# Optimization experiments

Measured on AMD Instinct MI355X. Metric: run time of the kernel, lower is better.

## Reference

```python
import jax, jax.numpy as jnp
import numpy as np


def setup_inputs() -> dict:
    key = jax.random.key(0)
    k1, k2 = jax.random.split(key)
    B, C, L = 64, 36, 4096
    x0 = jax.random.normal(k1, (B, C, L), dtype=jnp.float32)
    y0 = jax.random.normal(k2, (B, C, L), dtype=jnp.float32)
    return {"x0": x0, "y0": y0}


def reference(x0, y0):
    # Original torch code:
    #   result1 = (1/L) * sum_{i=0}^{L-1} roll(x0, i, dim=2) * y0
    #   result2 = (1/L) * sum_{i=0}^{L-1} roll(y0, i, dim=2) * y0
    # At each output position l, summing roll(x,i)[...,l] over all L shifts
    # visits every position of x exactly once, so the shift-sum equals the
    # full sum over the last axis. The loop is therefore mathematically
    # identical to:
    #   result1 = y0 * mean(x0, axis=-1, keepdims=True)
    #   result2 = y0 * mean(y0, axis=-1, keepdims=True)
    # which we compute in one fused pass (bit-for-bit same math up to
    # floating-point summation order).
    mean_x = jnp.mean(x0, axis=-1, keepdims=True)  # [B,C,1]
    mean_y = jnp.mean(y0, axis=-1, keepdims=True)  # [B,C,1]
    result = y0 * (mean_x + mean_y)                # [B,C,L]
    return result
```

## Files before the change

kernel.cpp:

```cpp
#include <hip/hip_runtime.h>
#include <stdint.h>


#define LL     4096
#define ROWS   (64 * 36)
#define BLOCK  64
#define F4LANE (LL / 4 / 64)

__global__ __launch_bounds__(BLOCK) void spo2_rowscale(
    const float* __restrict__ x,
    const float* __restrict__ y,
    float* __restrict__ out)
{
    const int lane = threadIdx.x;
    const size_t base = (size_t)blockIdx.x * LL;

    const float4* xv = (const float4*)(x + base);
    const float4* yv = (const float4*)(y + base);
    float4*       ov = (float4*)(out + base);

    float4 yr[F4LANE];
#pragma unroll
    for (int i = 0; i < F4LANE; ++i)
        yr[i] = yv[lane + i * 64];

    float sx0 = 0.f, sx1 = 0.f, sx2 = 0.f, sx3 = 0.f;
#pragma unroll
    for (int i = 0; i < F4LANE; i += 4) {
        float4 a = xv[lane + (i + 0) * 64];
        float4 b = xv[lane + (i + 1) * 64];
        float4 c = xv[lane + (i + 2) * 64];
        float4 d = xv[lane + (i + 3) * 64];
        sx0 += a.x + a.y + a.z + a.w;
        sx1 += b.x + b.y + b.z + b.w;
        sx2 += c.x + c.y + c.z + c.w;
        sx3 += d.x + d.y + d.z + d.w;
    }
    float s = (sx0 + sx1) + (sx2 + sx3);

    float sy0 = 0.f, sy1 = 0.f;
#pragma unroll
    for (int i = 0; i < F4LANE; i += 2) {
        sy0 += yr[i].x + yr[i].y + yr[i].z + yr[i].w;
        sy1 += yr[i + 1].x + yr[i + 1].y + yr[i + 1].z + yr[i + 1].w;
    }
    s += sy0 + sy1;

#pragma unroll
    for (int off = 32; off > 0; off >>= 1)
        s += __shfl_xor(s, off, 64);

    const float scale = s * (1.0f / (float)LL);

#pragma unroll
    for (int i = 0; i < F4LANE; ++i) {
        float4 o;
        o.x = yr[i].x * scale;
        o.y = yr[i].y * scale;
        o.z = yr[i].z * scale;
        o.w = yr[i].w * scale;
        ov[lane + i * 64] = o;
    }
}

extern "C" void kernel_launch(void* const* d_in, const int* in_sizes, int n_in,
                              void* d_out, int out_size, void* d_ws, size_t ws_size,
                              hipStream_t stream) {
    const float* x = (const float*)d_in[0];
    const float* y = (const float*)d_in[1];
    float* out = (float*)d_out;
    spo2_rowscale<<<ROWS, BLOCK, 0, stream>>>(x, y, out);
}
```

Baseline: 108.8 us.

## Use 256-thread blocks per row with LDS cross-wave reduction and nontemporal stores

Each row is now handled by four wavefronts (256 threads) instead of one, so each thread holds 4 float4s of x and y in registers instead of 16. A shared-memory step combines the per-wave partial sums, and the outputs are written with nontemporal stores. The intent is more memory-level parallelism and occupancy for this bandwidth-bound kernel, with less cache pollution from the output. In exchange it adds a __syncthreads and an LDS round trip per block.

```diff
diff --git a/kernel.cpp b/kernel.cpp
--- a/kernel.cpp
+++ b/kernel.cpp
@@ -2,64 +2,58 @@
 #include <stdint.h>
 
 
-#define LL     4096
-#define ROWS   (64 * 36)
-#define BLOCK  64
-#define F4LANE (LL / 4 / 64)
+typedef float v4f __attribute__((ext_vector_type(4)));
 
-__global__ __launch_bounds__(BLOCK) void spo2_rowscale(
+#define LL    4096
+#define ROWS  (64 * 36)
+#define BLOCK 256
+#define F4T   (LL / 4 / BLOCK)
+
+__global__ __launch_bounds__(BLOCK, 8) void spo2_rowscale(
     const float* __restrict__ x,
     const float* __restrict__ y,
     float* __restrict__ out)
 {
-    const int lane = threadIdx.x;
+    const int tid  = threadIdx.x;
     const size_t base = (size_t)blockIdx.x * LL;
 
-    const float4* xv = (const float4*)(x + base);
-    const float4* yv = (const float4*)(y + base);
-    float4*       ov = (float4*)(out + base);
+    const v4f* xv = (const v4f*)(x + base);
+    const v4f* yv = (const v4f*)(y + base);
+    v4f*       ov = (v4f*)(out + base);
 
-    float4 yr[F4LANE];
+    v4f xr[F4T], yr[F4T];
 #pragma unroll
-    for (int i = 0; i < F4LANE; ++i)
-        yr[i] = yv[lane + i * 64];
+    for (int i = 0; i < F4T; ++i) xr[i] = xv[tid + i * BLOCK];
+#pragma unroll
+    for (int i = 0; i < F4T; ++i) yr[i] = yv[tid + i * BLOCK];
 
-    float sx0 = 0.f, sx1 = 0.f, sx2 = 0.f, sx3 = 0.f;
+    float sx = 0.f, sy = 0.f;
 #pragma unroll
-    for (int i = 0; i < F4LANE; i += 4) {
-        float4 a = xv[lane + (i + 0) * 64];
-        float4 b = xv[lane + (i + 1) * 64];
-        float4 c = xv[lane + (i + 2) * 64];
-        float4 d = xv[lane + (i + 3) * 64];
-        sx0 += a.x + a.y + a.z + a.w;
-        sx1 += b.x + b.y + b.z + b.w;
-        sx2 += c.x + c.y + c.z + c.w;
-        sx3 += d.x + d.y + d.z + d.w;
+    for (int i = 0; i < F4T; ++i) {
+        sx += xr[i].x + xr[i].y + xr[i].z + xr[i].w;
+        sy += yr[i].x + yr[i].y + yr[i].z + yr[i].w;
     }
-    float s = (sx0 + sx1) + (sx2 + sx3);
-
-    float sy0 = 0.f, sy1 = 0.f;
-#pragma unroll
-    for (int i = 0; i < F4LANE; i += 2) {
-        sy0 += yr[i].x + yr[i].y + yr[i].z + yr[i].w;
-        sy1 += yr[i + 1].x + yr[i + 1].y + yr[i + 1].z + yr[i + 1].w;
-    }
-    s += sy0 + sy1;
+    float s = sx + sy;
 
 #pragma unroll
     for (int off = 32; off > 0; off >>= 1)
         s += __shfl_xor(s, off, 64);
 
-    const float scale = s * (1.0f / (float)LL);
+    __shared__ float rs[BLOCK / 64];
+    const int wid  = tid >> 6;
+    const int lane = tid & 63;
+    if (lane == 0) rs[wid] = s;
+    __syncthreads();
+
+    float total = 0.f;
+#pragma unroll
+    for (int w = 0; w < BLOCK / 64; ++w) total += rs[w];
+    const float scale = total * (1.0f / (float)LL);
 
 #pragma unroll
-    for (int i = 0; i < F4LANE; ++i) {
-        float4 o;
-        o.x = yr[i].x * scale;
-        o.y = yr[i].y * scale;
-        o.z = yr[i].z * scale;
-        o.w = yr[i].w * scale;
-        ov[lane + i * 64] = o;
+    for (int i = 0; i < F4T; ++i) {
+        v4f o = yr[i] * scale;
+        __builtin_nontemporal_store(o, ov + tid + i * BLOCK);
     }
 }
 
```

After: 107.1 us. No clear change (-1.6%).
